# Optimization experiments

Measured on AMD Instinct MI355X. Metric: run time of the kernel, lower is better.

The kernel has to match this reference:

```python
import jax, jax.numpy as jnp
import numpy as np

HIDDEN = 64
NUM_LAYERS = 3
EPS = 1e-5


def setup_inputs() -> dict:
    key = jax.random.key(0)
    ks = jax.random.split(key, 16)
    N, E, F_IN, H, C = 100000, 3200000, 12, HIDDEN, 2
    x = jax.random.normal(ks[0], (N, F_IN), dtype=jnp.float32)
    edge_index = jax.random.randint(ks[1], (2, E), 0, N, dtype=jnp.int64)
    s = lambda k, sh, fan: jax.random.normal(k, sh, dtype=jnp.float32) / np.sqrt(fan)
    return {
        "x": x,
        "edge_index": edge_index,
        "W_in": s(ks[2], (F_IN, H), F_IN),
        "b_in": jnp.zeros((H,), jnp.float32),
        "W_g": s(ks[3], (NUM_LAYERS, H, H), H),
        "b_g": jnp.zeros((NUM_LAYERS, H), jnp.float32),
        "gamma": jnp.ones((NUM_LAYERS, H), jnp.float32),
        "beta": jnp.zeros((NUM_LAYERS, H), jnp.float32),
        "W_c1": s(ks[4], (H, H // 2), H),
        "b_c1": jnp.zeros((H // 2,), jnp.float32),
        "W_c2": s(ks[5], (H // 2, C), H // 2),
        "b_c2": jnp.zeros((C,), jnp.float32),
    }


def _gcn_norm(edge_index, N):
    # GCNConv default: add self loops, symmetric normalization D^-1/2 (A+I) D^-1/2
    src, dst = edge_index[0], edge_index[1]
    deg = jax.ops.segment_sum(jnp.ones_like(dst, jnp.float32), dst, num_segments=N) + 1.0
    dinv = jax.lax.rsqrt(deg)
    norm_e = dinv[src] * dinv[dst]          # [E] per-edge coefficient
    self_norm = dinv * dinv                 # [N] self-loop coefficient
    return src, dst, norm_e, self_norm


def _gcn_layer(h, W, b, src, dst, norm_e, self_norm, N):
    h = h @ W                                # [N, H] linear transform first
    agg = jax.ops.segment_sum(h[src] * norm_e[:, None], dst, num_segments=N)
    return agg + h * self_norm[:, None] + b


def _batchnorm(h, gamma, beta):
    mu = jnp.mean(h, axis=0)
    var = jnp.mean(jnp.square(h - mu), axis=0)  # biased, as torch BN
    return (h - mu) * jax.lax.rsqrt(var + EPS) * gamma + beta


def reference(x, edge_index, W_in, b_in, W_g, b_g, gamma, beta, W_c1, b_c1, W_c2, b_c2):
    N = x.shape[0]
    src, dst, norm_e, self_norm = _gcn_norm(edge_index, N)
    h = jax.nn.relu(x @ W_in + b_in)
    for i in range(NUM_LAYERS):
        h = _gcn_layer(h, W_g[i], b_g[i], src, dst, norm_e, self_norm, N)
        h = _batchnorm(h, gamma[i], beta[i])
        if i < NUM_LAYERS - 1:
            h = jax.nn.relu(h)  # dropout omitted (inference/deterministic)
    h = jax.nn.relu(h @ W_c1 + b_c1)
    return h @ W_c2 + b_c2
```

## Files before the change

### kernel.cpp

```cpp
#include <hip/hip_runtime.h>

#define EPSV 1e-5f
#define BSH 8
#define BSZ 256
#define SB 104

__device__ inline float blo(unsigned u) { return __uint_as_float(u << 16); }
__device__ inline float bhi(unsigned u) { return __uint_as_float(u & 0xFFFF0000u); }
__device__ inline unsigned rne16(float v) {
    unsigned u = __float_as_uint(v);
    return (u + 0x7FFFu + ((u >> 16) & 1u)) >> 16;
}
__device__ inline unsigned pk(float lo, float hi) {
    return (rne16(hi) << 16) | rne16(lo);
}


__global__ __launch_bounds__(256) void k_hist(const int* __restrict__ dst,
                                              int* __restrict__ bcount, int E) {
    __shared__ int hist[1024];
    int t = threadIdx.x;
#pragma unroll
    for (int i = 0; i < 4; i++) hist[t + 256 * i] = 0;
    __syncthreads();
    int e0 = blockIdx.x * 4096;
#pragma unroll
    for (int r = 0; r < 16; r++) {
        int e = e0 + r * 256 + t;
        if (e < E) atomicAdd(&hist[dst[e] >> BSH], 1);
    }
    __syncthreads();
#pragma unroll
    for (int i = 0; i < 4; i++) {
        int bk = t + 256 * i;
        int h = hist[bk];
        if (h) atomicAdd(&bcount[bk], h);
    }
}

__global__ __launch_bounds__(256) void k_bscan(const int* __restrict__ bcount,
                                               int* __restrict__ bstart,
                                               int* __restrict__ gcur, int NB) {
    int t = threadIdx.x;
    int base = t * 4;
    int c[4], s = 0;
#pragma unroll
    for (int i = 0; i < 4; i++) {
        c[i] = (base + i < NB) ? bcount[base + i] : 0;
        s += c[i];
    }
    __shared__ int ls[256];
    ls[t] = s;
    __syncthreads();
    for (int off = 1; off < 256; off <<= 1) {
        int x = (t >= off) ? ls[t - off] : 0;
        __syncthreads();
        ls[t] += x;
        __syncthreads();
    }
    int run = (t == 0) ? 0 : ls[t - 1];
#pragma unroll
    for (int i = 0; i < 4; i++) {
        bstart[base + i] = run;
        gcur[base + i] = run;
        run += c[i];
    }
    if (t == 255) bstart[1024] = ls[255];
}

__global__ __launch_bounds__(256) void k_split(const int* __restrict__ src,
                                               const int* __restrict__ dst,
                                               int* __restrict__ gcur,
                                               unsigned* __restrict__ pairs, int E) {
    __shared__ int hist[1024];
    __shared__ int gb[1024];
    int t = threadIdx.x;
    int e0 = blockIdx.x * 4096;
    int sreg[16], dreg[16];
#pragma unroll
    for (int i = 0; i < 4; i++) hist[t + 256 * i] = 0;
    __syncthreads();
#pragma unroll
    for (int r = 0; r < 16; r++) {
        int e = e0 + r * 256 + t;
        if (e < E) {
            sreg[r] = src[e];
            dreg[r] = dst[e];
            atomicAdd(&hist[dreg[r] >> BSH], 1);
        } else {
            dreg[r] = -1;
        }
    }
    __syncthreads();
#pragma unroll
    for (int i = 0; i < 4; i++) {
        int bk = t + 256 * i;
        int h = hist[bk];
        gb[bk] = h ? atomicAdd(&gcur[bk], h) : 0;
    }
    __syncthreads();
#pragma unroll
    for (int i = 0; i < 4; i++) hist[t + 256 * i] = 0;
    __syncthreads();
#pragma unroll
    for (int r = 0; r < 16; r++) {
        if (dreg[r] >= 0) {
            int bk = dreg[r] >> BSH;
            int rk = atomicAdd(&hist[bk], 1);
            pairs[gb[bk] + rk] = ((unsigned)(dreg[r] & (BSZ - 1)) << 22) |
                                 (unsigned)sreg[r];
        }
    }
}

__global__ __launch_bounds__(256) void k_build(const unsigned* __restrict__ pairs,
                                               const int* __restrict__ bstart,
                                               int* __restrict__ rowptr,
                                               int* __restrict__ rowend,
                                               float* __restrict__ dinv,
                                               int* __restrict__ colidx, int N) {
    int bid = blockIdx.x, t = threadIdx.x;
    int n0 = bid << BSH;
    int e0 = bstart[bid], e1 = bstart[bid + 1];
    __shared__ int cnt[256];
    __shared__ int ls[256];
    __shared__ int cur[256];
    cnt[t] = 0;
    __syncthreads();
    for (int e = e0 + t; e < e1; e += 256)
        atomicAdd(&cnt[pairs[e] >> 22], 1);
    __syncthreads();
    ls[t] = cnt[t];
    __syncthreads();
    for (int off = 1; off < 256; off <<= 1) {
        int x = (t >= off) ? ls[t - off] : 0;
        __syncthreads();
        ls[t] += x;
        __syncthreads();
    }
    int start = e0 + ((t == 0) ? 0 : ls[t - 1]);
    cur[t] = start;
    int node = n0 + t;
    if (node < N) {
        rowptr[node] = start;
        rowend[node] = start + cnt[t];
        dinv[node] = rsqrtf((float)cnt[t] + 1.0f);
    }
    __syncthreads();
    for (int e = e0 + t; e < e1; e += 256) {
        unsigned p = pairs[e];
        int r = atomicAdd(&cur[p >> 22], 1);
        colidx[r] = (int)(p & 0x3FFFFFu);
    }
}


__global__ __launch_bounds__(256) void k_gemm0(const float* __restrict__ x,
                                               const float* __restrict__ Win,
                                               const float* __restrict__ bin,
                                               const float* __restrict__ W,
                                               const float* __restrict__ dinv,
                                               unsigned short* __restrict__ hl, int N) {
    __shared__ float zbuf[4][64];
    int wv = threadIdx.x >> 6;
    int j = threadIdx.x & 63;
    float w[64];
#pragma unroll
    for (int k = 0; k < 64; k++) w[k] = W[k * 64 + j];
    float wi[12];
#pragma unroll
    for (int k = 0; k < 12; k++) wi[k] = Win[k * 64 + j];
    float bj = bin[j];
    const float4* zr = (const float4*)&zbuf[wv][0];
    int wave = (blockIdx.x * 256 + threadIdx.x) >> 6;
    int nw = (gridDim.x * 256) >> 6;
    for (int node = wave; node < N; node += nw) {
        const float* xr = x + node * 12;
        float z = bj;
#pragma unroll
        for (int k = 0; k < 12; k++) z = fmaf(xr[k], wi[k], z);
        zbuf[wv][j] = fmaxf(z, 0.0f);
        asm volatile("s_waitcnt lgkmcnt(0)" ::: "memory");
        float acc = 0.0f;
#pragma unroll
        for (int kk = 0; kk < 16; kk++) {
            float4 z4 = zr[kk];
            acc = fmaf(z4.x, w[4 * kk + 0], acc);
            acc = fmaf(z4.y, w[4 * kk + 1], acc);
            acc = fmaf(z4.z, w[4 * kk + 2], acc);
            acc = fmaf(z4.w, w[4 * kk + 3], acc);
        }
        hl[node * 64 + j] = (unsigned short)rne16(acc * dinv[node]);
    }
}

__global__ __launch_bounds__(256) void k_gemmn(const float* __restrict__ W,
                                               const float* __restrict__ ab,
                                               const float* __restrict__ dinv,
                                               const unsigned* __restrict__ h2,
                                               unsigned short* __restrict__ hl, int N) {
    __shared__ float zbuf[4][64];
    int wv = threadIdx.x >> 6;
    int j = threadIdx.x & 63;
    float w[64];
#pragma unroll
    for (int k = 0; k < 64; k++) w[k] = W[k * 64 + j];
    float Aj = ab[j], Bj = ab[64 + j];
    const float4* zr = (const float4*)&zbuf[wv][0];
    int wave = (blockIdx.x * 256 + threadIdx.x) >> 6;
    int nw = (gridDim.x * 256) >> 6;
    for (int node = wave; node < N; node += nw) {
        unsigned u = h2[node * 32 + (j >> 1)];
        float h = (j & 1) ? bhi(u) : blo(u);
        zbuf[wv][j] = fmaxf(fmaf(Aj, h, Bj), 0.0f);
        asm volatile("s_waitcnt lgkmcnt(0)" ::: "memory");
        float acc = 0.0f;
#pragma unroll
        for (int kk = 0; kk < 16; kk++) {
            float4 z4 = zr[kk];
            acc = fmaf(z4.x, w[4 * kk + 0], acc);
            acc = fmaf(z4.y, w[4 * kk + 1], acc);
            acc = fmaf(z4.z, w[4 * kk + 2], acc);
            acc = fmaf(z4.w, w[4 * kk + 3], acc);
        }
        hl[node * 64 + j] = (unsigned short)rne16(acc * dinv[node]);
    }
}

__global__ __launch_bounds__(256) void k_agg(const int* __restrict__ rowptr,
                                             const int* __restrict__ rowend,
                                             const int* __restrict__ colidx,
                                             const float* __restrict__ dinv,
                                             const unsigned* __restrict__ hl2,
                                             const float* __restrict__ b,
                                             unsigned* __restrict__ out2, int N) {
    int t = threadIdx.x;
    int hw = t >> 5;
    int lane = t & 31;
    int sub = lane >> 3;
    int q = lane & 7;
    int d = blockIdx.x * 8 + hw;
    if (d >= N) return;
    int e0 = rowptr[d], e1 = rowend[d];
    const uint4* H = (const uint4*)hl2;

    float a0 = 0.f, a1 = 0.f, a2 = 0.f, a3 = 0.f;
    float a4 = 0.f, a5 = 0.f, a6 = 0.f, a7 = 0.f;
    float c0 = 0.f, c1 = 0.f, c2 = 0.f, c3 = 0.f;
    float c4 = 0.f, c5 = 0.f, c6 = 0.f, c7 = 0.f;

    if (sub == 0) {
        uint4 su = H[d * 8 + q];
        a0 = blo(su.x); a1 = bhi(su.x);
        a2 = blo(su.y); a3 = bhi(su.y);
        a4 = blo(su.z); a5 = bhi(su.z);
        a6 = blo(su.w); a7 = bhi(su.w);
    }

    int e = e0 + sub;
    for (; e + 12 < e1; e += 16) {
        int s0 = colidx[e];
        int s1 = colidx[e + 4];
        int s2 = colidx[e + 8];
        int s3 = colidx[e + 12];
        uint4 u0 = H[s0 * 8 + q];
        uint4 u1 = H[s1 * 8 + q];
        uint4 u2 = H[s2 * 8 + q];
        uint4 u3 = H[s3 * 8 + q];
        a0 += blo(u0.x); a1 += bhi(u0.x); a2 += blo(u0.y); a3 += bhi(u0.y);
        a4 += blo(u0.z); a5 += bhi(u0.z); a6 += blo(u0.w); a7 += bhi(u0.w);
        c0 += blo(u1.x); c1 += bhi(u1.x); c2 += blo(u1.y); c3 += bhi(u1.y);
        c4 += blo(u1.z); c5 += bhi(u1.z); c6 += blo(u1.w); c7 += bhi(u1.w);
        a0 += blo(u2.x); a1 += bhi(u2.x); a2 += blo(u2.y); a3 += bhi(u2.y);
        a4 += blo(u2.z); a5 += bhi(u2.z); a6 += blo(u2.w); a7 += bhi(u2.w);
        c0 += blo(u3.x); c1 += bhi(u3.x); c2 += blo(u3.y); c3 += bhi(u3.y);
        c4 += blo(u3.z); c5 += bhi(u3.z); c6 += blo(u3.w); c7 += bhi(u3.w);
    }
    for (; e < e1; e += 4) {
        uint4 u = H[colidx[e] * 8 + q];
        a0 += blo(u.x); a1 += bhi(u.x); a2 += blo(u.y); a3 += bhi(u.y);
        a4 += blo(u.z); a5 += bhi(u.z); a6 += blo(u.w); a7 += bhi(u.w);
    }
    a0 += c0; a1 += c1; a2 += c2; a3 += c3;
    a4 += c4; a5 += c5; a6 += c6; a7 += c7;

    a0 += __shfl_xor(a0, 8);  a0 += __shfl_xor(a0, 16);
    a1 += __shfl_xor(a1, 8);  a1 += __shfl_xor(a1, 16);
    a2 += __shfl_xor(a2, 8);  a2 += __shfl_xor(a2, 16);
    a3 += __shfl_xor(a3, 8);  a3 += __shfl_xor(a3, 16);
    a4 += __shfl_xor(a4, 8);  a4 += __shfl_xor(a4, 16);
    a5 += __shfl_xor(a5, 8);  a5 += __shfl_xor(a5, 16);
    a6 += __shfl_xor(a6, 8);  a6 += __shfl_xor(a6, 16);
    a7 += __shfl_xor(a7, 8);  a7 += __shfl_xor(a7, 16);

    if (sub == 0) {
        float dv = dinv[d];
        int fb = q * 8;
        float o0 = fmaf(a0, dv, b[fb + 0]);
        float o1 = fmaf(a1, dv, b[fb + 1]);
        float o2 = fmaf(a2, dv, b[fb + 2]);
        float o3 = fmaf(a3, dv, b[fb + 3]);
        float o4 = fmaf(a4, dv, b[fb + 4]);
        float o5 = fmaf(a5, dv, b[fb + 5]);
        float o6 = fmaf(a6, dv, b[fb + 6]);
        float o7 = fmaf(a7, dv, b[fb + 7]);
        uint4 o;
        o.x = pk(o0, o1);
        o.y = pk(o2, o3);
        o.z = pk(o4, o5);
        o.w = pk(o6, o7);
        ((uint4*)out2)[d * 8 + q] = o;
    }
}

__global__ __launch_bounds__(256) void k_stats(const unsigned* __restrict__ h2,
                                               float* __restrict__ part, int N) {
    int t = threadIdx.x;
    int hw = t >> 5, f = t & 31;
    float s0 = 0.f, s1 = 0.f, q0 = 0.f, q1 = 0.f;
    for (int node = blockIdx.x * 8 + hw; node < N; node += gridDim.x * 8) {
        unsigned u = h2[node * 32 + f];
        float r0 = blo(u), r1 = bhi(u);
        s0 += r0; q0 = fmaf(r0, r0, q0);
        s1 += r1; q1 = fmaf(r1, r1, q1);
    }
    __shared__ float rs[8][64];
    __shared__ float rq[8][64];
    rs[hw][2 * f] = s0; rs[hw][2 * f + 1] = s1;
    rq[hw][2 * f] = q0; rq[hw][2 * f + 1] = q1;
    __syncthreads();
    if (t < 128) {
        float acc = 0.f;
#pragma unroll
        for (int h = 0; h < 8; h++) acc += (t < 64) ? rs[h][t] : rq[h][t - 64];
        part[blockIdx.x * 128 + t] = acc;
    }
}

__global__ __launch_bounds__(128) void k_red(const float* __restrict__ part,
                                             const float* __restrict__ gamma,
                                             const float* __restrict__ beta,
                                             float* __restrict__ ab, int nb, float invN) {
    int t = threadIdx.x;
    float a = 0.f, b2 = 0.f, c = 0.f, d = 0.f;
    for (int i = 0; i < nb; i += 4) {
        a += part[i * 128 + t];
        b2 += part[(i + 1) * 128 + t];
        c += part[(i + 2) * 128 + t];
        d += part[(i + 3) * 128 + t];
    }
    __shared__ float sm[128];
    sm[t] = (a + b2) + (c + d);
    __syncthreads();
    if (t < 64) {
        float mu = sm[t] * invN;
        float var = fmaf(-mu, mu, sm[t + 64] * invN);
        float A = rsqrtf(var + EPSV) * gamma[t];
        ab[t] = A;
        ab[64 + t] = fmaf(-mu, A, beta[t]);
    }
}

__global__ __launch_bounds__(256) void k_cls(const unsigned* __restrict__ h2,
                                             const float* __restrict__ ab,
                                             const float* __restrict__ W1,
                                             const float* __restrict__ b1,
                                             const float* __restrict__ W2,
                                             const float* __restrict__ b2,
                                             float* __restrict__ out, int N) {
    int lane = threadIdx.x & 63;
    int half = lane >> 5, jj = lane & 31;
    float w[64];
    float bj = b1[jj];
#pragma unroll
    for (int k = 0; k < 64; k++) {
        float w1 = W1[k * 32 + jj];
        w[k] = ab[k] * w1;
        bj = fmaf(ab[64 + k], w1, bj);
    }
    float w20 = W2[jj * 2 + 0], w21 = W2[jj * 2 + 1];
    float b20 = b2[0], b21 = b2[1];
    int wave = (blockIdx.x * 256 + threadIdx.x) >> 6;
    int nw = (gridDim.x * 256) >> 6;
    for (int base = wave * 2; base < N; base += nw * 2) {
        int node = base + half;
        int vnode = node < N ? node : 0;
        const uint4* row = (const uint4*)(h2 + vnode * 32);
        float acc = bj;
#pragma unroll
        for (int kk = 0; kk < 8; kk++) {
            uint4 u = row[kk];
            acc = fmaf(blo(u.x), w[8 * kk + 0], acc);
            acc = fmaf(bhi(u.x), w[8 * kk + 1], acc);
            acc = fmaf(blo(u.y), w[8 * kk + 2], acc);
            acc = fmaf(bhi(u.y), w[8 * kk + 3], acc);
            acc = fmaf(blo(u.z), w[8 * kk + 4], acc);
            acc = fmaf(bhi(u.z), w[8 * kk + 5], acc);
            acc = fmaf(blo(u.w), w[8 * kk + 6], acc);
            acc = fmaf(bhi(u.w), w[8 * kk + 7], acc);
        }
        float hv = fmaxf(acc, 0.0f);
        float t0 = hv * w20, t1 = hv * w21;
#pragma unroll
        for (int m = 1; m <= 16; m <<= 1) {
            t0 += __shfl_xor(t0, m, 64);
            t1 += __shfl_xor(t1, m, 64);
        }
        if (jj == 0 && node < N) {
            ((float2*)out)[node] = make_float2(t0 + b20, t1 + b21);
        }
    }
}

extern "C" void kernel_launch(void* const* d_in, const int* in_sizes, int n_in,
                              void* d_out, int out_size, void* d_ws, size_t ws_size,
                              hipStream_t stream) {
    const float* x     = (const float*)d_in[0];
    const int*   ei    = (const int*)d_in[1];
    const float* Win   = (const float*)d_in[2];
    const float* bin   = (const float*)d_in[3];
    const float* Wg    = (const float*)d_in[4];
    const float* bg    = (const float*)d_in[5];
    const float* gamma = (const float*)d_in[6];
    const float* beta  = (const float*)d_in[7];
    const float* W1    = (const float*)d_in[8];
    const float* b1    = (const float*)d_in[9];
    const float* W2    = (const float*)d_in[10];
    const float* b2    = (const float*)d_in[11];
    float* out = (float*)d_out;

    int N = in_sizes[0] / 12;
    int E = in_sizes[1] / 2;
    const int* src = ei;
    const int* dst = ei + E;
    float invN = 1.0f / (float)N;
    int NB = (N + BSZ - 1) >> BSH;

    char* ws = (char*)d_ws;
    size_t szhin = ((size_t)N * 64 * 2 + 255) / 256 * 256;
    size_t szE4  = ((size_t)E * 4 + 255) / 256 * 256;
    size_t szN4  = ((size_t)N * 4 + 255) / 256 * 256;

    size_t off = 0;
    unsigned* hin2     = (unsigned*)(ws + off); off += szhin;
    unsigned short* hl = (unsigned short*)(ws + off); off += szhin;
    int* colidx        = (int*)(ws + off); off += szE4;
    int* rowptr        = (int*)(ws + off); off += szN4;
    int* rowend        = (int*)(ws + off); off += szN4;
    float* dinv        = (float*)(ws + off); off += szN4;
    int* bcount        = (int*)(ws + off); off += 4096;
    int* bstart        = (int*)(ws + off); off += 8192;
    int* gcur          = (int*)(ws + off); off += 4096;
    float* part        = (float*)(ws + off); off += (size_t)SB * 128 * 4;
    float* ab          = (float*)(ws + off); off += 512;

    unsigned* pairs = (unsigned*)ws;
    size_t need = off;
    if (2 * szhin < (size_t)E * 4) {
        pairs = (unsigned*)(ws + off);
        need += (size_t)E * 4;
    }
    if (ws_size < need || NB > 1024 || N >= (1 << 22)) return;

    hipMemsetAsync(bcount, 0, 4096, stream);

    int EB = (E + 4095) / 4096;
    k_hist<<<EB, 256, 0, stream>>>(dst, bcount, E);
    k_bscan<<<1, 256, 0, stream>>>(bcount, bstart, gcur, NB);
    k_split<<<EB, 256, 0, stream>>>(src, dst, gcur, pairs, E);
    k_build<<<NB, 256, 0, stream>>>(pairs, bstart, rowptr, rowend, dinv, colidx, N);

    int AB = (N + 7) / 8;
    for (int i = 0; i < 3; i++) {
        if (i == 0)
            k_gemm0<<<2048, 256, 0, stream>>>(x, Win, bin, Wg, dinv, hl, N);
        else
            k_gemmn<<<2048, 256, 0, stream>>>(Wg + i * 64 * 64, ab, dinv, hin2,
                                              hl, N);
        k_agg<<<AB, 256, 0, stream>>>(rowptr, rowend, colidx, dinv,
                                      (const unsigned*)hl, bg + i * 64, hin2, N);
        k_stats<<<SB, 256, 0, stream>>>(hin2, part, N);
        k_red<<<1, 128, 0, stream>>>(part, gamma + i * 64, beta + i * 64, ab,
                                     SB, invN);
    }
    k_cls<<<1024, 256, 0, stream>>>(hin2, ab, W1, b1, W2, b2, out, N);
}
```

Measured before the change: 565.7 us.

## Fuse BN stats and reduction via atomics, prefetch GEMM inputs, split classifier accumulators

Merges the per-layer stats and single-block reduce kernels into one kernel. It accumulates per-feature sums with global atomics and uses a last-block ticket to compute the BN scale and shift. It also raises the stats grid size, unrolls the stats loop four ways, software-prefetches the next node's inputs in both GEMM kernels, and splits the classifier dot product into four independent accumulators with a launch-bounds occupancy hint. The aim is to cut launch count and latency stalls, at the cost of atomic contention and nondeterministic float summation order.

```diff
diff --git a/kernel.cpp b/kernel.cpp
--- a/kernel.cpp
+++ b/kernel.cpp
@@ -3,7 +3,7 @@
 #define EPSV 1e-5f
 #define BSH 8
 #define BSZ 256
-#define SB 104
+#define SBR 416
 
 __device__ inline float blo(unsigned u) { return __uint_as_float(u << 16); }
 __device__ inline float bhi(unsigned u) { return __uint_as_float(u & 0xFFFF0000u); }
@@ -174,11 +174,22 @@
     const float4* zr = (const float4*)&zbuf[wv][0];
     int wave = (blockIdx.x * 256 + threadIdx.x) >> 6;
     int nw = (gridDim.x * 256) >> 6;
-    for (int node = wave; node < N; node += nw) {
-        const float* xr = x + node * 12;
+    int node = wave;
+    float xa[12];
+    if (node < N) {
+        const float* xr = x + (size_t)node * 12;
+#pragma unroll
+        for (int k = 0; k < 12; k++) xa[k] = xr[k];
+    }
+    for (; node < N; node += nw) {
+        int nxt = node + nw;
+        float xb[12];
+        const float* xr2 = x + (size_t)(nxt < N ? nxt : node) * 12;
+#pragma unroll
+        for (int k = 0; k < 12; k++) xb[k] = xr2[k];
         float z = bj;
 #pragma unroll
-        for (int k = 0; k < 12; k++) z = fmaf(xr[k], wi[k], z);
+        for (int k = 0; k < 12; k++) z = fmaf(xa[k], wi[k], z);
         zbuf[wv][j] = fmaxf(z, 0.0f);
         asm volatile("s_waitcnt lgkmcnt(0)" ::: "memory");
         float acc = 0.0f;
@@ -190,7 +201,9 @@
             acc = fmaf(z4.z, w[4 * kk + 2], acc);
             acc = fmaf(z4.w, w[4 * kk + 3], acc);
         }
-        hl[node * 64 + j] = (unsigned short)rne16(acc * dinv[node]);
+        hl[(size_t)node * 64 + j] = (unsigned short)rne16(acc * dinv[node]);
+#pragma unroll
+        for (int k = 0; k < 12; k++) xa[k] = xb[k];
     }
 }
 
@@ -209,8 +222,11 @@
     const float4* zr = (const float4*)&zbuf[wv][0];
     int wave = (blockIdx.x * 256 + threadIdx.x) >> 6;
     int nw = (gridDim.x * 256) >> 6;
-    for (int node = wave; node < N; node += nw) {
-        unsigned u = h2[node * 32 + (j >> 1)];
+    int node = wave;
+    unsigned u = (node < N) ? h2[(size_t)node * 32 + (j >> 1)] : 0u;
+    for (; node < N; node += nw) {
+        int nxt = node + nw;
+        unsigned unext = h2[(size_t)(nxt < N ? nxt : node) * 32 + (j >> 1)];
         float h = (j & 1) ? bhi(u) : blo(u);
         zbuf[wv][j] = fmaxf(fmaf(Aj, h, Bj), 0.0f);
         asm volatile("s_waitcnt lgkmcnt(0)" ::: "memory");
@@ -223,7 +239,8 @@
             acc = fmaf(z4.z, w[4 * kk + 2], acc);
             acc = fmaf(z4.w, w[4 * kk + 3], acc);
         }
-        hl[node * 64 + j] = (unsigned short)rne16(acc * dinv[node]);
+        hl[(size_t)node * 64 + j] = (unsigned short)rne16(acc * dinv[node]);
+        u = unext;
     }
 }
 
@@ -313,19 +330,42 @@
     }
 }
 
-__global__ __launch_bounds__(256) void k_stats(const unsigned* __restrict__ h2,
-                                               float* __restrict__ part, int N) {
+__global__ __launch_bounds__(256) void k_statsred(const unsigned* __restrict__ h2,
+                                                  float* __restrict__ ps,
+                                                  int* __restrict__ ticket,
+                                                  const float* __restrict__ gamma,
+                                                  const float* __restrict__ beta,
+                                                  float* __restrict__ ab,
+                                                  int N, float invN) {
     int t = threadIdx.x;
     int hw = t >> 5, f = t & 31;
     float s0 = 0.f, s1 = 0.f, q0 = 0.f, q1 = 0.f;
-    for (int node = blockIdx.x * 8 + hw; node < N; node += gridDim.x * 8) {
-        unsigned u = h2[node * 32 + f];
-        float r0 = blo(u), r1 = bhi(u);
-        s0 += r0; q0 = fmaf(r0, r0, q0);
-        s1 += r1; q1 = fmaf(r1, r1, q1);
+    int stride = gridDim.x << 3;
+    int n = blockIdx.x * 8 + hw;
+    for (; n + 3 * stride < N; n += stride << 2) {
+        unsigned ua = h2[(size_t)n * 32 + f];
+        unsigned ub = h2[((size_t)n + stride) * 32 + f];
+        unsigned uc = h2[((size_t)n + 2 * stride) * 32 + f];
+        unsigned ud = h2[((size_t)n + 3 * stride) * 32 + f];
+        float r;
+        r = blo(ua); s0 += r; q0 = fmaf(r, r, q0);
+        r = bhi(ua); s1 += r; q1 = fmaf(r, r, q1);
+        r = blo(ub); s0 += r; q0 = fmaf(r, r, q0);
+        r = bhi(ub); s1 += r; q1 = fmaf(r, r, q1);
+        r = blo(uc); s0 += r; q0 = fmaf(r, r, q0);
+        r = bhi(uc); s1 += r; q1 = fmaf(r, r, q1);
+        r = blo(ud); s0 += r; q0 = fmaf(r, r, q0);
+        r = bhi(ud); s1 += r; q1 = fmaf(r, r, q1);
+    }
+    for (; n < N; n += stride) {
+        unsigned u = h2[(size_t)n * 32 + f];
+        float r;
+        r = blo(u); s0 += r; q0 = fmaf(r, r, q0);
+        r = bhi(u); s1 += r; q1 = fmaf(r, r, q1);
     }
     __shared__ float rs[8][64];
     __shared__ float rq[8][64];
+    __shared__ int lastflag;
     rs[hw][2 * f] = s0; rs[hw][2 * f + 1] = s1;
     rq[hw][2 * f] = q0; rq[hw][2 * f + 1] = q1;
     __syncthreads();
@@ -333,41 +373,32 @@
         float acc = 0.f;
 #pragma unroll
         for (int h = 0; h < 8; h++) acc += (t < 64) ? rs[h][t] : rq[h][t - 64];
-        part[blockIdx.x * 128 + t] = acc;
-    }
-}
-
-__global__ __launch_bounds__(128) void k_red(const float* __restrict__ part,
-                                             const float* __restrict__ gamma,
-                                             const float* __restrict__ beta,
-                                             float* __restrict__ ab, int nb, float invN) {
-    int t = threadIdx.x;
-    float a = 0.f, b2 = 0.f, c = 0.f, d = 0.f;
-    for (int i = 0; i < nb; i += 4) {
-        a += part[i * 128 + t];
-        b2 += part[(i + 1) * 128 + t];
-        c += part[(i + 2) * 128 + t];
-        d += part[(i + 3) * 128 + t];
-    }
-    __shared__ float sm[128];
-    sm[t] = (a + b2) + (c + d);
-    __syncthreads();
-    if (t < 64) {
-        float mu = sm[t] * invN;
-        float var = fmaf(-mu, mu, sm[t + 64] * invN);
+        atomicAdd(&ps[t], acc);
+    }
+    __syncthreads();
+    if (t == 0) {
+        __threadfence();
+        lastflag = (atomicAdd(ticket, 1) == (int)gridDim.x - 1);
+    }
+    __syncthreads();
+    if (lastflag && t < 64) {
+        float S = atomicAdd(&ps[t], 0.0f);
+        float Q = atomicAdd(&ps[64 + t], 0.0f);
+        float mu = S * invN;
+        float var = fmaf(-mu, mu, Q * invN);
         float A = rsqrtf(var + EPSV) * gamma[t];
         ab[t] = A;
         ab[64 + t] = fmaf(-mu, A, beta[t]);
     }
 }
 
-__global__ __launch_bounds__(256) void k_cls(const unsigned* __restrict__ h2,
-                                             const float* __restrict__ ab,
-                                             const float* __restrict__ W1,
-                                             const float* __restrict__ b1,
-                                             const float* __restrict__ W2,
-                                             const float* __restrict__ b2,
-                                             float* __restrict__ out, int N) {
+__global__ __launch_bounds__(256, 2) void k_cls(const unsigned* __restrict__ h2,
+                                                const float* __restrict__ ab,
+                                                const float* __restrict__ W1,
+                                                const float* __restrict__ b1,
+                                                const float* __restrict__ W2,
+                                                const float* __restrict__ b2,
+                                                float* __restrict__ out, int N) {
     int lane = threadIdx.x & 63;
     int half = lane >> 5, jj = lane & 31;
     float w[64];
@@ -386,19 +417,20 @@
         int node = base + half;
         int vnode = node < N ? node : 0;
         const uint4* row = (const uint4*)(h2 + vnode * 32);
-        float acc = bj;
+        float A0 = bj, A1 = 0.f, A2 = 0.f, A3 = 0.f;
 #pragma unroll
         for (int kk = 0; kk < 8; kk++) {
             uint4 u = row[kk];
-            acc = fmaf(blo(u.x), w[8 * kk + 0], acc);
-            acc = fmaf(bhi(u.x), w[8 * kk + 1], acc);
-            acc = fmaf(blo(u.y), w[8 * kk + 2], acc);
-            acc = fmaf(bhi(u.y), w[8 * kk + 3], acc);
-            acc = fmaf(blo(u.z), w[8 * kk + 4], acc);
-            acc = fmaf(bhi(u.z), w[8 * kk + 5], acc);
-            acc = fmaf(blo(u.w), w[8 * kk + 6], acc);
-            acc = fmaf(bhi(u.w), w[8 * kk + 7], acc);
-        }
+            A0 = fmaf(blo(u.x), w[8 * kk + 0], A0);
+            A1 = fmaf(bhi(u.x), w[8 * kk + 1], A1);
+            A2 = fmaf(blo(u.y), w[8 * kk + 2], A2);
+            A3 = fmaf(bhi(u.y), w[8 * kk + 3], A3);
+            A0 = fmaf(blo(u.z), w[8 * kk + 4], A0);
+            A1 = fmaf(bhi(u.z), w[8 * kk + 5], A1);
+            A2 = fmaf(blo(u.w), w[8 * kk + 6], A2);
+            A3 = fmaf(bhi(u.w), w[8 * kk + 7], A3);
+        }
+        float acc = (A0 + A1) + (A2 + A3);
         float hv = fmaxf(acc, 0.0f);
         float t0 = hv * w20, t1 = hv * w21;
 #pragma unroll
@@ -449,9 +481,11 @@
     int* rowend        = (int*)(ws + off); off += szN4;
     float* dinv        = (float*)(ws + off); off += szN4;
     int* bcount        = (int*)(ws + off); off += 4096;
+    float* ps3         = (float*)(ws + off); off += 3 * 512;
+    int* tick          = (int*)(ws + off); off += 16;
+    size_t msz = 4096 + 3 * 512 + 16;
     int* bstart        = (int*)(ws + off); off += 8192;
     int* gcur          = (int*)(ws + off); off += 4096;
-    float* part        = (float*)(ws + off); off += (size_t)SB * 128 * 4;
     float* ab          = (float*)(ws + off); off += 512;
 
     unsigned* pairs = (unsigned*)ws;
@@ -462,7 +496,7 @@
     }
     if (ws_size < need || NB > 1024 || N >= (1 << 22)) return;
 
-    hipMemsetAsync(bcount, 0, 4096, stream);
+    hipMemsetAsync(bcount, 0, msz, stream);
 
     int EB = (E + 4095) / 4096;
     k_hist<<<EB, 256, 0, stream>>>(dst, bcount, E);
@@ -479,9 +513,9 @@
                                               hl, N);
         k_agg<<<AB, 256, 0, stream>>>(rowptr, rowend, colidx, dinv,
                                       (const unsigned*)hl, bg + i * 64, hin2, N);
-        k_stats<<<SB, 256, 0, stream>>>(hin2, part, N);
-        k_red<<<1, 128, 0, stream>>>(part, gamma + i * 64, beta + i * 64, ab,
-                                     SB, invN);
+        k_statsred<<<SBR, 256, 0, stream>>>(hin2, ps3 + i * 128, tick + i,
+                                            gamma + i * 64, beta + i * 64, ab,
+                                            N, invN);
     }
     k_cls<<<1024, 256, 0, stream>>>(hin2, ab, W1, b1, W2, b2, out, N);
 }
```

New measurement: 481.6 us. -14.9%, faster.
